# Optimization experiments

Measured on AMD Instinct MI355X. Metric: run time of the kernel, lower is better.

The kernel has to match this reference:

```python
import jax, jax.numpy as jnp
import numpy as np

# ---- batched 6-qubit state-vector simulator ----

def _apply_b(state, gate, wire):
    # per-sample gate: gate (B,2,2), state (B,)+(2,)*w
    B = state.shape[0]; w = state.ndim - 1
    pre = 2 ** wire; post = 2 ** (w - wire - 1)
    s = state.reshape(B, pre, 2, post)
    s = jnp.einsum('bij,bpjq->bpiq', gate, s)
    return s.reshape(state.shape)

def _apply_s(state, gate, wire):
    # shared gate: gate (2,2)
    B = state.shape[0]; w = state.ndim - 1
    pre = 2 ** wire; post = 2 ** (w - wire - 1)
    s = state.reshape(B, pre, 2, post)
    s = jnp.einsum('ij,bpjq->bpiq', gate, s)
    return s.reshape(state.shape)

def _cnot(state, ctrl, tgt):
    s0 = jnp.take(state, 0, axis=1 + ctrl)
    s1 = jnp.take(state, 1, axis=1 + ctrl)
    t_ax = 1 + tgt if tgt < ctrl else tgt  # target axis after removing ctrl axis
    s1 = jnp.flip(s1, axis=t_ax)
    return jnp.stack([s0, s1], axis=1 + ctrl)

def _ry(t):
    c = jnp.cos(t / 2); s = jnp.sin(t / 2)
    return jnp.stack([jnp.stack([c, -s], -1), jnp.stack([s, c], -1)], -2).astype(jnp.complex64)

def _rz(t):
    e = jnp.exp(-0.5j * t.astype(jnp.complex64))
    z = jnp.zeros_like(e)
    return jnp.stack([jnp.stack([e, z], -1), jnp.stack([z, jnp.conj(e)], -1)], -2)

def _rx(t):
    c = jnp.cos(t / 2).astype(jnp.complex64)
    s = (-1j * jnp.sin(t / 2)).astype(jnp.complex64)
    return jnp.stack([jnp.stack([c, s], -1), jnp.stack([s, c], -1)], -2)

def _expvals_z(state):
    p = state.real ** 2 + state.imag ** 2  # (B,)+(2,)*w probabilities
    w = state.ndim - 1
    outs = []
    for i in range(w):
        axes = tuple(a for a in range(1, w + 1) if a != i + 1)
        m = p.sum(axis=axes)  # (B,2) marginal on wire i
        outs.append(m[:, 0] - m[:, 1])
    return jnp.stack(outs, axis=1)  # (B, w) -- matches torch.stack(outputs).T

def _circuit(x, weights):
    # x: (B, w) rescaled features, weights: (layers, 3*w)
    B, w = x.shape
    layers = weights.shape[0]
    e1 = jnp.arctan(x)        # featue_function_1
    e2 = jnp.arctan(x * x)    # featue_function_2 ('atan' type)
    state = jnp.zeros((B,) + (2,) * w, jnp.complex64).at[(slice(None),) + (0,) * w].set(1.0)
    for i in range(w):
        state = _apply_b(state, _ry(e1[:, i]), i)  # AngleEmbedding rotation='Y'
    for i in range(w):
        state = _apply_b(state, _rz(e2[:, i]), i)  # AngleEmbedding rotation='Z'
    for l in range(layers):
        for i in range(w):
            state = _cnot(state, i, (i + 1) % w)
        for i in range(w):
            state = _cnot(state, i, (i + 2) % w)
        for i in range(w):
            state = _apply_s(state, _rx(weights[l, 3 * i + 0]), i)
            state = _apply_s(state, _ry(weights[l, 3 * i + 1]), i)
            state = _apply_s(state, _rz(weights[l, 3 * i + 2]), i)
    return _expvals_z(state)

def _forward(x, phi, Wc, bc):
    Bsz = x.shape[0]
    w = Wc.shape[0]
    sig = jax.nn.sigmoid

    def step(carry, x_t):
        c, h = carry
        z = jnp.concatenate([x_t, h], axis=1)          # torch.hstack([input[:,i], h])
        X = 2.0 * sig(z @ Wc.T + bc) - 1.0             # feature_combiner + rescale
        f_t = sig(_circuit(X, phi[0]))
        i_t = sig(_circuit(X, phi[1]))
        C_t = sig(_circuit(X, phi[2]))
        o_t = sig(_circuit(X, phi[3]))
        c_new = f_t * c + i_t * C_t
        rescaled = o_t * jnp.tanh(c_new)
        h_new = _circuit(rescaled, phi[4])
        y_t = _circuit(rescaled, phi[5])
        return (c_new, h_new), y_t

    init = (jnp.zeros((Bsz, w), jnp.float32), jnp.zeros((Bsz, w), jnp.float32))
    (c, h), ys = jax.lax.scan(jax.checkpoint(step), init, jnp.swapaxes(x, 0, 1))
    return jnp.swapaxes(ys, 0, 1), c, h  # y_out (B,T,w), (c, h)

def setup_inputs() -> dict:
    key = jax.random.key(0)
    k1, k2, k3, k4 = jax.random.split(key, 4)
    x = jax.random.normal(k1, (512, 256, 8), jnp.float32)
    phi = jax.random.normal(k2, (6, 2, 18), jnp.float32) / jnp.sqrt(jnp.float32(2.0))  # std 1/sqrt(layers)
    bound = float(1.0 / np.sqrt(8 + 6))  # Linear(feature_dim+wires, wires) default init
    Wc = jax.random.uniform(k3, (6, 14), jnp.float32, -bound, bound)
    bc = jax.random.uniform(k4, (6,), jnp.float32, -bound, bound)
    return {"x": x, "phi": phi, "Wc": Wc, "bc": bc}

def reference(x, phi, Wc, bc):
    return _forward(x, phi, Wc, bc)
```

## Files before the change

### kernel.cpp

```cpp
#include <hip/hip_runtime.h>


namespace {

constexpr int BATCH  = 512;
constexpr int TSTEPS = 256;

typedef float v2f __attribute__((ext_vector_type(2)));

__device__ __forceinline__ v2f splat2(float s) { v2f r; r.x = s; r.y = s; return r; }
__device__ __forceinline__ v2f cswapneg(v2f v) { v2f r; r.x = -v.y; r.y = v.x; return r; }

__device__ __forceinline__ float sigf(float v) { return 1.0f / (1.0f + __expf(-v)); }
__device__ __forceinline__ float tanh_fast(float v) { return 1.0f - 2.0f / (1.0f + __expf(v + v)); }

__device__ __forceinline__ float rl(float v, int l) {
  return __int_as_float(__builtin_amdgcn_readlane(__float_as_int(v), l));
}

template<int CTRL>
__device__ __forceinline__ float dppmov(float v) {
  return __int_as_float(__builtin_amdgcn_mov_dpp(__float_as_int(v), CTRL, 0xF, 0xF, true));
}

template<int M>
__device__ __forceinline__ float shx(float v, int lane4) {
  if constexpr      (M == 0x01) return dppmov<0xB1>(v);
  else if constexpr (M == 0x02) return dppmov<0x4E>(v);
  else if constexpr (M == 0x03) return dppmov<0x1B>(v);
  else if constexpr (M == 0x04) return dppmov<0x1B>(dppmov<0x141>(v));
  else if constexpr (M == 0x05) return dppmov<0x4E>(dppmov<0x141>(v));
  else if constexpr (M == 0x07) return dppmov<0x141>(v);
  else if constexpr (M == 0x08) return dppmov<0x128>(v);
  else if constexpr (M == 0x0A) return dppmov<0x4E>(dppmov<0x128>(v));
  else if constexpr (M == 0x0C) return dppmov<0x1B>(dppmov<0x140>(v));
  else if constexpr (M == 0x0F) return dppmov<0x140>(v);
  else if constexpr (M < 32) {
    return __int_as_float(__builtin_amdgcn_ds_swizzle(__float_as_int(v), 0x1F | (M << 10)));
  } else {
    return __int_as_float(__builtin_amdgcn_ds_bpermute(lane4 ^ (M << 2), __float_as_int(v)));
  }
}

template<int M>
__device__ __forceinline__ void gate1(v2f& s, float4 A, int pm, int lane4) {
  v2f v; v.x = shx<M>(s.x, lane4); v.y = shx<M>(s.y, lane4);
  float sai = __int_as_float(__float_as_int(A.y) ^ pm);
  float sbr = __int_as_float(__float_as_int(A.z) ^ pm);
  v2f u = splat2(A.x) * s;
  u = __builtin_elementwise_fma(splat2(sai), cswapneg(s), u);
  u = __builtin_elementwise_fma(splat2(sbr), v,           u);
  u = __builtin_elementwise_fma(splat2(A.w), cswapneg(v), u);
  s = u;
}

__device__ __forceinline__ void gate_chain(v2f& s, const float4 (&CA)[12],
                                           const int (&pm)[12], int lane4) {
  gate1<0x0F>(s, CA[0],  pm[0],  lane4);
  gate1<0x1E>(s, CA[1],  pm[1],  lane4);
  gate1<0x3C>(s, CA[2],  pm[2],  lane4);
  gate1<0x3B>(s, CA[3],  pm[3],  lane4);
  gate1<0x3F>(s, CA[4],  pm[4],  lane4);
  gate1<0x3D>(s, CA[5],  pm[5],  lane4);
  gate1<0x16>(s, CA[6],  pm[6],  lane4);
  gate1<0x26>(s, CA[7],  pm[7],  lane4);
  gate1<0x05>(s, CA[8],  pm[8],  lane4);
  gate1<0x28>(s, CA[9],  pm[9],  lane4);
  gate1<0x14>(s, CA[10], pm[10], lane4);
  gate1<0x0A>(s, CA[11], pm[11], lane4);
}

__device__ __forceinline__ float expvals(v2f s, const float (&fs)[9],
                                         int lane4, int gaddr) {
  float p  = fmaf(s.x, s.x, s.y * s.y);
  float pa = shx<1>(p, lane4), pb = shx<2>(p, lane4), pc = shx<3>(p, lane4);
  p = fmaf(fs[0], p, fmaf(fs[1], pa, fmaf(fs[2], pb, pc)));
  pa = shx<4>(p, lane4); pb = shx<8>(p, lane4); pc = shx<12>(p, lane4);
  p = fmaf(fs[3], p, fmaf(fs[4], pa, fmaf(fs[5], pb, pc)));
  pa = shx<16>(p, lane4); pb = shx<32>(p, lane4); pc = shx<48>(p, lane4);
  p = fmaf(fs[6], p, fmaf(fs[7], pa, fmaf(fs[8], pb, pc)));
  return __int_as_float(__builtin_amdgcn_ds_bpermute(gaddr, __float_as_int(p)));
}

__device__ __forceinline__ void trig(float Xv, float& A_, float& B_, float& C_, float& D_) {
  float tq   = Xv * Xv;
  float cth1 = rsqrtf(1.f + tq);
  float sth1 = Xv * cth1;
  float u1   = 1.f + cth1, r1 = rsqrtf(u1 + u1);
  float c1   = u1 * r1,    s1 = sth1 * r1;
  float tq2  = tq * tq;
  float cth2 = rsqrtf(1.f + tq2);
  float sth2 = tq * cth2;
  float u2   = 1.f + cth2, r2 = rsqrtf(u2 + u2);
  float c2   = u2 * r2,    s2 = sth2 * r2;
  A_ = c1 * c2; B_ = c1 * s2; C_ = s1 * c2; D_ = s1 * s2;
}

__device__ __forceinline__ v2f embed_rl(float A_, float B_, float C_, float D_, int lane) {
  float ar, ai;
  {
    float Aj = rl(A_,0), Bj = rl(B_,0), Cj = rl(C_,0), Dj = rl(D_,0);
    bool bj = lane & 1;
    ar = bj ? Cj : Aj;
    ai = bj ? Dj : -Bj;
  }
#pragma unroll
  for (int jj = 1; jj < 6; ++jj) {
    float Aj = rl(A_,jj), Bj = rl(B_,jj), Cj = rl(C_,jj), Dj = rl(D_,jj);
    bool bj = (lane >> jj) & 1;
    float fr = bj ? Cj : Aj;
    float fi = bj ? Dj : -Bj;
    float nr = ar * fr - ai * fi;
    ai = fmaf(ar, fi, ai * fr);
    ar = nr;
  }
  v2f s; s.x = ar; s.y = ai; return s;
}

#define PACK_IDX ((0x2AULL)|(0x15ULL<<6)|(0x01ULL<<12)|(0x35ULL<<18)|(0x3AULL<<24)|(0x3DULL<<30))
#define PIN4(v) asm volatile("" : "+v"((v).x), "+v"((v).y), "+v"((v).z), "+v"((v).w))

}

__global__ __attribute__((amdgpu_flat_work_group_size(256, 256)))
           __attribute__((amdgpu_waves_per_eu(2, 2)))
void qlstm_kernel(const float* __restrict__ x, const float* __restrict__ phi,
                  const float* __restrict__ Wc, const float* __restrict__ bc,
                  float* __restrict__ out)
{
  __shared__ float4 fG[72];
  __shared__ float4 gates4[6];
  __shared__ __align__(16) float h_s[8];

  const int tid   = threadIdx.x;
  const int wave  = tid >> 6;
  const int lane  = tid & 63;
  const int lane4 = lane << 2;
  const int b     = blockIdx.x;

  if (tid < 72) {
    int g = tid / 12, rem = tid % 12, l = rem / 6, i = rem % 6;
    const float* w = phi + g*36 + l*18 + i*3;
    float sa, ca, sb, cb, sc, cc;
    sincosf(0.5f * w[0], &sa, &ca);
    sincosf(0.5f * w[1], &sb, &cb);
    sincosf(0.5f * w[2], &sc, &cc);
    float m00r =  cb*ca, m00i =  sb*sa;
    float m01r = -sb*ca, m01i = -cb*sa;
    float4 A;
    A.x = m00r*cc + m00i*sc;  A.y = m00i*cc - m00r*sc;
    A.z = m01r*cc + m01i*sc;  A.w = m01i*cc - m01r*sc;
    fG[tid] = A;
  }
  if (tid < 8) h_s[tid] = 0.f;
  __syncthreads();

  const int j = (lane < 6) ? lane : 0;
  float Wr[14];
#pragma unroll
  for (int k = 0; k < 14; ++k) Wr[k] = Wc[j*14 + k];
  const float bcj = bc[j];

  float sgn[6];
#pragma unroll
  for (int k = 0; k < 6; ++k) sgn[k] = ((lane >> k) & 1) ? -1.f : 1.f;
  float fs[9] = { sgn[0]*sgn[1], sgn[1], sgn[0],
                  sgn[2]*sgn[3], sgn[3], sgn[2],
                  sgn[4]*sgn[5], sgn[5], sgn[4] };

  int sh    = (lane < 6) ? (6 * lane) : 0;
  int gaddr = (int)((PACK_IDX >> sh) & 63ULL) << 2;

  constexpr unsigned BM[2][6] = {
    {0x18,0x30,0x39,0x0C,0x26,0x33},
    {0x2A,0x15,0x01,0x35,0x3A,0x3D}};
  int pm[12];
#pragma unroll
  for (int l = 0; l < 2; ++l)
#pragma unroll
    for (int i = 0; i < 6; ++i)
      pm[l*6+i] = (__popc(lane & (int)BM[l][i]) & 1) << 31;
#pragma unroll
  for (int g = 0; g < 12; ++g) asm volatile("" : "+v"(pm[g]));

  float4 CA1[12], CA2[12];
#pragma unroll
  for (int i = 0; i < 12; ++i) {
    CA1[i] = fG[wave * 12 + i];
    CA2[i] = fG[(4 + (wave & 1)) * 12 + i];
  }
#pragma unroll
  for (int i = 0; i < 12; ++i) { PIN4(CA1[i]); PIN4(CA2[i]); }

  float c_sc  = 0.f;
  float hlast = 0.f;

  const float* xbase = x + (size_t)b * TSTEPS * 8;
  float4 xa = *(const float4*)(xbase);
  float4 xb = *(const float4*)(xbase + 4);

  for (int t = 0; t < TSTEPS; ++t) {
    float4 h4 = *(const float4*)&h_s[0];
    float2 h2 = *(const float2*)&h_s[4];
    float acc = bcj;
    acc = fmaf(xa.x, Wr[0],  acc); acc = fmaf(xa.y, Wr[1],  acc);
    acc = fmaf(xa.z, Wr[2],  acc); acc = fmaf(xa.w, Wr[3],  acc);
    acc = fmaf(xb.x, Wr[4],  acc); acc = fmaf(xb.y, Wr[5],  acc);
    acc = fmaf(xb.z, Wr[6],  acc); acc = fmaf(xb.w, Wr[7],  acc);
    acc = fmaf(h4.x, Wr[8],  acc); acc = fmaf(h4.y, Wr[9],  acc);
    acc = fmaf(h4.z, Wr[10], acc); acc = fmaf(h4.w, Wr[11], acc);
    acc = fmaf(h2.x, Wr[12], acc); acc = fmaf(h2.y, Wr[13], acc);
    float Xj = 1.f - 2.f / (1.f + __expf(acc));

    int tn = (t + 1 < TSTEPS) ? (t + 1) : t;
    float4 xa_n = *(const float4*)(xbase + (size_t)tn * 8);
    float4 xb_n = *(const float4*)(xbase + (size_t)tn * 8 + 4);

    float A_, B_, C_, D_;
    trig(Xj, A_, B_, C_, D_);
    v2f s = embed_rl(A_, B_, C_, D_, lane);
    gate_chain(s, CA1, pm, lane4);
    float Wv  = expvals(s, fs, lane4, gaddr);
    float sgv = sigf(Wv);
    if (lane < 6) ((float*)&gates4[lane])[wave] = sgv;
    __syncthreads();

    if (wave < 2) {
      float4 g4 = gates4[j];
      float cn  = fmaf(g4.x, c_sc, g4.y * g4.z);
      c_sc = cn;
      float resc = g4.w * tanh_fast(cn);
      float A2, B2, C2, D2;
      trig(resc, A2, B2, C2, D2);
      v2f s2 = embed_rl(A2, B2, C2, D2, lane);
      gate_chain(s2, CA2, pm, lane4);
      float Wv2 = expvals(s2, fs, lane4, gaddr);
      if (wave == 0) {
        if (lane < 6) h_s[lane] = Wv2;
        hlast = Wv2;
      } else if (lane < 6) {
        out[((size_t)b * TSTEPS + t) * 6 + lane] = Wv2;
      }
    }
    xa = xa_n; xb = xb_n;
    __syncthreads();
  }

  if (wave == 0 && lane < 6) {
    size_t cbase = (size_t)BATCH * TSTEPS * 6;
    out[cbase + (size_t)b * 6 + lane] = c_sc;
    out[cbase + (size_t)BATCH * 6 + (size_t)b * 6 + lane] = hlast;
  }
}

extern "C" void kernel_launch(void* const* d_in, const int* in_sizes, int n_in,
                              void* d_out, int out_size, void* d_ws, size_t ws_size,
                              hipStream_t stream) {
  const float* x   = (const float*)d_in[0];
  const float* phi = (const float*)d_in[1];
  const float* Wc  = (const float*)d_in[2];
  const float* bc  = (const float*)d_in[3];
  float* out = (float*)d_out;
  (void)in_sizes; (void)n_in; (void)out_size; (void)d_ws; (void)ws_size;
  hipLaunchKernelGGL(qlstm_kernel, dim3(BATCH), dim3(256), 0, stream,
                     x, phi, Wc, bc, out);
}
```

Baseline: 622.6 us.

## Run all six circuits per sample in one wave with interleaved gate chains

Each batch element now uses a single 64-lane wavefront instead of four waves. That wave runs the four gate circuits interleaved (N=4), then the two output circuits interleaved (N=2). Gate coefficients are read from LDS in a gate-major layout, and the hidden state stays in registers and is broadcast with readlane. This removes the two block-wide barriers and the LDS exchange per timestep, and gives the scheduler independent chains to hide shuffle latency. In exchange each wave does all six circuits serially, only 512 waves run in total, and coefficients are reloaded from LDS every step instead of held pinned in registers.

```diff
diff --git a/kernel.cpp b/kernel.cpp
--- a/kernel.cpp
+++ b/kernel.cpp
@@ -42,44 +42,71 @@
   }
 }
 
-template<int M>
-__device__ __forceinline__ void gate1(v2f& s, float4 A, int pm, int lane4) {
-  v2f v; v.x = shx<M>(s.x, lane4); v.y = shx<M>(s.y, lane4);
-  float sai = __int_as_float(__float_as_int(A.y) ^ pm);
-  float sbr = __int_as_float(__float_as_int(A.z) ^ pm);
-  v2f u = splat2(A.x) * s;
-  u = __builtin_elementwise_fma(splat2(sai), cswapneg(s), u);
-  u = __builtin_elementwise_fma(splat2(sbr), v,           u);
-  u = __builtin_elementwise_fma(splat2(A.w), cswapneg(v), u);
-  s = u;
-}
-
-__device__ __forceinline__ void gate_chain(v2f& s, const float4 (&CA)[12],
-                                           const int (&pm)[12], int lane4) {
-  gate1<0x0F>(s, CA[0],  pm[0],  lane4);
-  gate1<0x1E>(s, CA[1],  pm[1],  lane4);
-  gate1<0x3C>(s, CA[2],  pm[2],  lane4);
-  gate1<0x3B>(s, CA[3],  pm[3],  lane4);
-  gate1<0x3F>(s, CA[4],  pm[4],  lane4);
-  gate1<0x3D>(s, CA[5],  pm[5],  lane4);
-  gate1<0x16>(s, CA[6],  pm[6],  lane4);
-  gate1<0x26>(s, CA[7],  pm[7],  lane4);
-  gate1<0x05>(s, CA[8],  pm[8],  lane4);
-  gate1<0x28>(s, CA[9],  pm[9],  lane4);
-  gate1<0x14>(s, CA[10], pm[10], lane4);
-  gate1<0x0A>(s, CA[11], pm[11], lane4);
-}
-
-__device__ __forceinline__ float expvals(v2f s, const float (&fs)[9],
-                                         int lane4, int gaddr) {
-  float p  = fmaf(s.x, s.x, s.y * s.y);
-  float pa = shx<1>(p, lane4), pb = shx<2>(p, lane4), pc = shx<3>(p, lane4);
-  p = fmaf(fs[0], p, fmaf(fs[1], pa, fmaf(fs[2], pb, pc)));
-  pa = shx<4>(p, lane4); pb = shx<8>(p, lane4); pc = shx<12>(p, lane4);
-  p = fmaf(fs[3], p, fmaf(fs[4], pa, fmaf(fs[5], pb, pc)));
-  pa = shx<16>(p, lane4); pb = shx<32>(p, lane4); pc = shx<48>(p, lane4);
-  p = fmaf(fs[6], p, fmaf(fs[7], pa, fmaf(fs[8], pb, pc)));
-  return __int_as_float(__builtin_amdgcn_ds_bpermute(gaddr, __float_as_int(p)));
+template<int M, int N>
+__device__ __forceinline__ void gateN(v2f (&s)[N], const float4* __restrict__ Ks,
+                                      int pm, int lane4) {
+  float4 A[N];
+#pragma unroll
+  for (int c = 0; c < N; ++c) A[c] = Ks[c];
+  v2f v[N];
+#pragma unroll
+  for (int c = 0; c < N; ++c) {
+    v[c].x = shx<M>(s[c].x, lane4);
+    v[c].y = shx<M>(s[c].y, lane4);
+  }
+#pragma unroll
+  for (int c = 0; c < N; ++c) {
+    float sai = __int_as_float(__float_as_int(A[c].y) ^ pm);
+    float sbr = __int_as_float(__float_as_int(A[c].z) ^ pm);
+    v2f u = splat2(A[c].x) * s[c];
+    u = __builtin_elementwise_fma(splat2(sai), cswapneg(s[c]), u);
+    u = __builtin_elementwise_fma(splat2(sbr), v[c],           u);
+    u = __builtin_elementwise_fma(splat2(A[c].w), cswapneg(v[c]), u);
+    s[c] = u;
+  }
+}
+
+template<int N>
+__device__ __forceinline__ void chainN(v2f (&s)[N], const float4* __restrict__ Kt,
+                                       int base, const int (&pm)[12], int lane4) {
+  gateN<0x0F, N>(s, Kt + 0*6  + base, pm[0],  lane4);
+  gateN<0x1E, N>(s, Kt + 1*6  + base, pm[1],  lane4);
+  gateN<0x3C, N>(s, Kt + 2*6  + base, pm[2],  lane4);
+  gateN<0x3B, N>(s, Kt + 3*6  + base, pm[3],  lane4);
+  gateN<0x3F, N>(s, Kt + 4*6  + base, pm[4],  lane4);
+  gateN<0x3D, N>(s, Kt + 5*6  + base, pm[5],  lane4);
+  gateN<0x16, N>(s, Kt + 6*6  + base, pm[6],  lane4);
+  gateN<0x26, N>(s, Kt + 7*6  + base, pm[7],  lane4);
+  gateN<0x05, N>(s, Kt + 8*6  + base, pm[8],  lane4);
+  gateN<0x28, N>(s, Kt + 9*6  + base, pm[9],  lane4);
+  gateN<0x14, N>(s, Kt + 10*6 + base, pm[10], lane4);
+  gateN<0x0A, N>(s, Kt + 11*6 + base, pm[11], lane4);
+}
+
+template<int N>
+__device__ __forceinline__ void expvalsN(const v2f (&s)[N], float (&Wv)[N],
+                                         const float (&fs)[9], int lane4, int gaddr) {
+  float p[N];
+#pragma unroll
+  for (int c = 0; c < N; ++c) p[c] = fmaf(s[c].x, s[c].x, s[c].y * s[c].y);
+#pragma unroll
+  for (int c = 0; c < N; ++c) {
+    float pa = shx<1>(p[c], lane4), pb = shx<2>(p[c], lane4), pc = shx<3>(p[c], lane4);
+    p[c] = fmaf(fs[0], p[c], fmaf(fs[1], pa, fmaf(fs[2], pb, pc)));
+  }
+#pragma unroll
+  for (int c = 0; c < N; ++c) {
+    float pa = shx<4>(p[c], lane4), pb = shx<8>(p[c], lane4), pc = shx<12>(p[c], lane4);
+    p[c] = fmaf(fs[3], p[c], fmaf(fs[4], pa, fmaf(fs[5], pb, pc)));
+  }
+#pragma unroll
+  for (int c = 0; c < N; ++c) {
+    float pa = shx<16>(p[c], lane4), pb = shx<32>(p[c], lane4), pc = shx<48>(p[c], lane4);
+    p[c] = fmaf(fs[6], p[c], fmaf(fs[7], pa, fmaf(fs[8], pb, pc)));
+  }
+#pragma unroll
+  for (int c = 0; c < N; ++c)
+    Wv[c] = __int_as_float(__builtin_amdgcn_ds_bpermute(gaddr, __float_as_int(p[c])));
 }
 
 __device__ __forceinline__ void trig(float Xv, float& A_, float& B_, float& C_, float& D_) {
@@ -118,28 +145,22 @@
 }
 
 #define PACK_IDX ((0x2AULL)|(0x15ULL<<6)|(0x01ULL<<12)|(0x35ULL<<18)|(0x3AULL<<24)|(0x3DULL<<30))
-#define PIN4(v) asm volatile("" : "+v"((v).x), "+v"((v).y), "+v"((v).z), "+v"((v).w))
-
-}
-
-__global__ __attribute__((amdgpu_flat_work_group_size(256, 256)))
-           __attribute__((amdgpu_waves_per_eu(2, 2)))
+
+}
+
+__global__ __launch_bounds__(64) __attribute__((amdgpu_waves_per_eu(1)))
 void qlstm_kernel(const float* __restrict__ x, const float* __restrict__ phi,
                   const float* __restrict__ Wc, const float* __restrict__ bc,
                   float* __restrict__ out)
 {
-  __shared__ float4 fG[72];
-  __shared__ float4 gates4[6];
-  __shared__ __align__(16) float h_s[8];
-
-  const int tid   = threadIdx.x;
-  const int wave  = tid >> 6;
-  const int lane  = tid & 63;
+  __shared__ float4 Kt[72];
+
+  const int lane  = threadIdx.x & 63;
   const int lane4 = lane << 2;
   const int b     = blockIdx.x;
 
-  if (tid < 72) {
-    int g = tid / 12, rem = tid % 12, l = rem / 6, i = rem % 6;
+  for (int k = lane; k < 72; k += 64) {
+    int g = k / 12, rem = k % 12, l = rem / 6, i = rem % 6;
     const float* w = phi + g*36 + l*18 + i*3;
     float sa, ca, sb, cb, sc, cc;
     sincosf(0.5f * w[0], &sa, &ca);
@@ -150,9 +171,8 @@
     float4 A;
     A.x = m00r*cc + m00i*sc;  A.y = m00i*cc - m00r*sc;
     A.z = m01r*cc + m01i*sc;  A.w = m01i*cc - m01r*sc;
-    fG[tid] = A;
-  }
-  if (tid < 8) h_s[tid] = 0.f;
+    Kt[rem*6 + g] = A;
+  }
   __syncthreads();
 
   const int j = (lane < 6) ? lane : 0;
@@ -180,36 +200,25 @@
 #pragma unroll
     for (int i = 0; i < 6; ++i)
       pm[l*6+i] = (__popc(lane & (int)BM[l][i]) & 1) << 31;
-#pragma unroll
-  for (int g = 0; g < 12; ++g) asm volatile("" : "+v"(pm[g]));
-
-  float4 CA1[12], CA2[12];
-#pragma unroll
-  for (int i = 0; i < 12; ++i) {
-    CA1[i] = fG[wave * 12 + i];
-    CA2[i] = fG[(4 + (wave & 1)) * 12 + i];
-  }
-#pragma unroll
-  for (int i = 0; i < 12; ++i) { PIN4(CA1[i]); PIN4(CA2[i]); }
-
-  float c_sc  = 0.f;
-  float hlast = 0.f;
+
+  float c_sc = 0.f;
+  float hreg = 0.f;
 
   const float* xbase = x + (size_t)b * TSTEPS * 8;
   float4 xa = *(const float4*)(xbase);
   float4 xb = *(const float4*)(xbase + 4);
 
   for (int t = 0; t < TSTEPS; ++t) {
-    float4 h4 = *(const float4*)&h_s[0];
-    float2 h2 = *(const float2*)&h_s[4];
+    float h0 = rl(hreg,0), h1 = rl(hreg,1), h2 = rl(hreg,2);
+    float h3 = rl(hreg,3), h4 = rl(hreg,4), h5 = rl(hreg,5);
     float acc = bcj;
     acc = fmaf(xa.x, Wr[0],  acc); acc = fmaf(xa.y, Wr[1],  acc);
     acc = fmaf(xa.z, Wr[2],  acc); acc = fmaf(xa.w, Wr[3],  acc);
     acc = fmaf(xb.x, Wr[4],  acc); acc = fmaf(xb.y, Wr[5],  acc);
     acc = fmaf(xb.z, Wr[6],  acc); acc = fmaf(xb.w, Wr[7],  acc);
-    acc = fmaf(h4.x, Wr[8],  acc); acc = fmaf(h4.y, Wr[9],  acc);
-    acc = fmaf(h4.z, Wr[10], acc); acc = fmaf(h4.w, Wr[11], acc);
-    acc = fmaf(h2.x, Wr[12], acc); acc = fmaf(h2.y, Wr[13], acc);
+    acc = fmaf(h0,   Wr[8],  acc); acc = fmaf(h1,   Wr[9],  acc);
+    acc = fmaf(h2,   Wr[10], acc); acc = fmaf(h3,   Wr[11], acc);
+    acc = fmaf(h4,   Wr[12], acc); acc = fmaf(h5,   Wr[13], acc);
     float Xj = 1.f - 2.f / (1.f + __expf(acc));
 
     int tn = (t + 1 < TSTEPS) ? (t + 1) : t;
@@ -218,38 +227,36 @@
 
     float A_, B_, C_, D_;
     trig(Xj, A_, B_, C_, D_);
-    v2f s = embed_rl(A_, B_, C_, D_, lane);
-    gate_chain(s, CA1, pm, lane4);
-    float Wv  = expvals(s, fs, lane4, gaddr);
-    float sgv = sigf(Wv);
-    if (lane < 6) ((float*)&gates4[lane])[wave] = sgv;
-    __syncthreads();
-
-    if (wave < 2) {
-      float4 g4 = gates4[j];
-      float cn  = fmaf(g4.x, c_sc, g4.y * g4.z);
-      c_sc = cn;
-      float resc = g4.w * tanh_fast(cn);
-      float A2, B2, C2, D2;
-      trig(resc, A2, B2, C2, D2);
-      v2f s2 = embed_rl(A2, B2, C2, D2, lane);
-      gate_chain(s2, CA2, pm, lane4);
-      float Wv2 = expvals(s2, fs, lane4, gaddr);
-      if (wave == 0) {
-        if (lane < 6) h_s[lane] = Wv2;
-        hlast = Wv2;
-      } else if (lane < 6) {
-        out[((size_t)b * TSTEPS + t) * 6 + lane] = Wv2;
-      }
-    }
+    v2f e = embed_rl(A_, B_, C_, D_, lane);
+    v2f s4[4] = { e, e, e, e };
+    chainN<4>(s4, Kt, 0, pm, lane4);
+    float Wv[4];
+    expvalsN<4>(s4, Wv, fs, lane4, gaddr);
+
+    float fg = sigf(Wv[0]), ig = sigf(Wv[1]);
+    float Cg = sigf(Wv[2]), og = sigf(Wv[3]);
+    float cn = fmaf(fg, c_sc, ig * Cg);
+    c_sc = cn;
+    float resc = og * tanh_fast(cn);
+
+    float A2, B2, C2, D2;
+    trig(resc, A2, B2, C2, D2);
+    v2f e2 = embed_rl(A2, B2, C2, D2, lane);
+    v2f s2[2] = { e2, e2 };
+    chainN<2>(s2, Kt, 4, pm, lane4);
+    float Wv2[2];
+    expvalsN<2>(s2, Wv2, fs, lane4, gaddr);
+
+    hreg = Wv2[0];
+    if (lane < 6) out[((size_t)b * TSTEPS + t) * 6 + lane] = Wv2[1];
+
     xa = xa_n; xb = xb_n;
-    __syncthreads();
-  }
-
-  if (wave == 0 && lane < 6) {
+  }
+
+  if (lane < 6) {
     size_t cbase = (size_t)BATCH * TSTEPS * 6;
     out[cbase + (size_t)b * 6 + lane] = c_sc;
-    out[cbase + (size_t)BATCH * 6 + (size_t)b * 6 + lane] = hlast;
+    out[cbase + (size_t)BATCH * 6 + (size_t)b * 6 + lane] = hreg;
   }
 }
 
@@ -262,6 +269,6 @@
   const float* bc  = (const float*)d_in[3];
   float* out = (float*)d_out;
   (void)in_sizes; (void)n_in; (void)out_size; (void)d_ws; (void)ws_size;
-  hipLaunchKernelGGL(qlstm_kernel, dim3(BATCH), dim3(256), 0, stream,
+  hipLaunchKernelGGL(qlstm_kernel, dim3(BATCH), dim3(64), 0, stream,
                      x, phi, Wc, bc, out);
 }
```

Measured after the change: 1.997 ms. +220.8%, slower.

## Drop final bpermute, build embedding as product tree, precompute gate coefficients

Applied to the files above, without the earlier changes.

Each sample's wire-j result is now read straight from the lane that already holds the reduced expectation, so the final ds_bpermute in expv goes away. Gate indices move to those specific lanes (gidx). The product-state embedding is built as a balanced tree of complex multiplies instead of a serial chain, which shortens the dependency chain. Gate matrices are computed once in a small prep kernel into workspace instead of in every block, at the cost of an extra launch and of dropping the register-pinning asm.

```diff
diff --git a/kernel.cpp b/kernel.cpp
--- a/kernel.cpp
+++ b/kernel.cpp
@@ -10,6 +10,9 @@
 
 __device__ __forceinline__ v2f splat2(float s) { v2f r; r.x = s; r.y = s; return r; }
 __device__ __forceinline__ v2f cswapneg(v2f v) { v2f r; r.x = -v.y; r.y = v.x; return r; }
+__device__ __forceinline__ v2f cmul(v2f a, v2f b) {
+  v2f r; r.x = fmaf(a.x, b.x, -(a.y * b.y)); r.y = fmaf(a.x, b.y, a.y * b.x); return r;
+}
 
 __device__ __forceinline__ float sigf(float v) { return 1.0f / (1.0f + __expf(-v)); }
 __device__ __forceinline__ float tanh_fast(float v) { return 1.0f - 2.0f / (1.0f + __expf(v + v)); }
@@ -54,24 +57,23 @@
   s = u;
 }
 
-__device__ __forceinline__ void gate_chain(v2f& s, const float4 (&CA)[12],
-                                           const int (&pm)[12], int lane4) {
-  gate1<0x0F>(s, CA[0],  pm[0],  lane4);
-  gate1<0x1E>(s, CA[1],  pm[1],  lane4);
-  gate1<0x3C>(s, CA[2],  pm[2],  lane4);
-  gate1<0x3B>(s, CA[3],  pm[3],  lane4);
-  gate1<0x3F>(s, CA[4],  pm[4],  lane4);
-  gate1<0x3D>(s, CA[5],  pm[5],  lane4);
-  gate1<0x16>(s, CA[6],  pm[6],  lane4);
-  gate1<0x26>(s, CA[7],  pm[7],  lane4);
-  gate1<0x05>(s, CA[8],  pm[8],  lane4);
-  gate1<0x28>(s, CA[9],  pm[9],  lane4);
-  gate1<0x14>(s, CA[10], pm[10], lane4);
-  gate1<0x0A>(s, CA[11], pm[11], lane4);
-}
-
-__device__ __forceinline__ float expvals(v2f s, const float (&fs)[9],
-                                         int lane4, int gaddr) {
+__device__ __forceinline__ void chain12(v2f& s, const float4 (&K)[12],
+                                        const int (&pm)[12], int lane4) {
+  gate1<0x0F>(s, K[0],  pm[0],  lane4);
+  gate1<0x1E>(s, K[1],  pm[1],  lane4);
+  gate1<0x3C>(s, K[2],  pm[2],  lane4);
+  gate1<0x3B>(s, K[3],  pm[3],  lane4);
+  gate1<0x3F>(s, K[4],  pm[4],  lane4);
+  gate1<0x3D>(s, K[5],  pm[5],  lane4);
+  gate1<0x16>(s, K[6],  pm[6],  lane4);
+  gate1<0x26>(s, K[7],  pm[7],  lane4);
+  gate1<0x05>(s, K[8],  pm[8],  lane4);
+  gate1<0x28>(s, K[9],  pm[9],  lane4);
+  gate1<0x14>(s, K[10], pm[10], lane4);
+  gate1<0x0A>(s, K[11], pm[11], lane4);
+}
+
+__device__ __forceinline__ float expv(v2f s, const float (&fs)[9], int lane4) {
   float p  = fmaf(s.x, s.x, s.y * s.y);
   float pa = shx<1>(p, lane4), pb = shx<2>(p, lane4), pc = shx<3>(p, lane4);
   p = fmaf(fs[0], p, fmaf(fs[1], pa, fmaf(fs[2], pb, pc)));
@@ -79,7 +81,7 @@
   p = fmaf(fs[3], p, fmaf(fs[4], pa, fmaf(fs[5], pb, pc)));
   pa = shx<16>(p, lane4); pb = shx<32>(p, lane4); pc = shx<48>(p, lane4);
   p = fmaf(fs[6], p, fmaf(fs[7], pa, fmaf(fs[8], pb, pc)));
-  return __int_as_float(__builtin_amdgcn_ds_bpermute(gaddr, __float_as_int(p)));
+  return p;
 }
 
 __device__ __forceinline__ void trig(float Xv, float& A_, float& B_, float& C_, float& D_) {
@@ -96,50 +98,29 @@
   A_ = c1 * c2; B_ = c1 * s2; C_ = s1 * c2; D_ = s1 * s2;
 }
 
-__device__ __forceinline__ v2f embed_rl(float A_, float B_, float C_, float D_, int lane) {
-  float ar, ai;
-  {
-    float Aj = rl(A_,0), Bj = rl(B_,0), Cj = rl(C_,0), Dj = rl(D_,0);
-    bool bj = lane & 1;
-    ar = bj ? Cj : Aj;
-    ai = bj ? Dj : -Bj;
-  }
-#pragma unroll
-  for (int jj = 1; jj < 6; ++jj) {
-    float Aj = rl(A_,jj), Bj = rl(B_,jj), Cj = rl(C_,jj), Dj = rl(D_,jj);
-    bool bj = (lane >> jj) & 1;
-    float fr = bj ? Cj : Aj;
-    float fi = bj ? Dj : -Bj;
-    float nr = ar * fr - ai * fi;
-    ai = fmaf(ar, fi, ai * fr);
-    ar = nr;
-  }
-  v2f s; s.x = ar; s.y = ai; return s;
-}
-
-#define PACK_IDX ((0x2AULL)|(0x15ULL<<6)|(0x01ULL<<12)|(0x35ULL<<18)|(0x3AULL<<24)|(0x3DULL<<30))
-#define PIN4(v) asm volatile("" : "+v"((v).x), "+v"((v).y), "+v"((v).z), "+v"((v).w))
-
-}
-
-__global__ __attribute__((amdgpu_flat_work_group_size(256, 256)))
-           __attribute__((amdgpu_waves_per_eu(2, 2)))
-void qlstm_kernel(const float* __restrict__ x, const float* __restrict__ phi,
-                  const float* __restrict__ Wc, const float* __restrict__ bc,
-                  float* __restrict__ out)
-{
-  __shared__ float4 fG[72];
-  __shared__ float4 gates4[6];
-  __shared__ __align__(16) float h_s[8];
-
-  const int tid   = threadIdx.x;
-  const int wave  = tid >> 6;
-  const int lane  = tid & 63;
-  const int lane4 = lane << 2;
-  const int b     = blockIdx.x;
-
-  if (tid < 72) {
-    int g = tid / 12, rem = tid % 12, l = rem / 6, i = rem % 6;
+__device__ __forceinline__ v2f embed_tree(float A_, float B_, float C_, float D_, int lane) {
+  constexpr int LW[6] = {0x2A, 0x15, 0x01, 0x35, 0x3A, 0x3D};
+  v2f f[6];
+#pragma unroll
+  for (int w = 0; w < 6; ++w) {
+    float Aj = rl(A_, LW[w]), Bj = rl(B_, LW[w]);
+    float Cj = rl(C_, LW[w]), Dj = rl(D_, LW[w]);
+    bool bj = (lane >> w) & 1;
+    f[w].x = bj ? Cj : Aj;
+    f[w].y = bj ? Dj : -Bj;
+  }
+  v2f p01 = cmul(f[0], f[1]);
+  v2f p23 = cmul(f[2], f[3]);
+  v2f p45 = cmul(f[4], f[5]);
+  return cmul(cmul(p01, p23), p45);
+}
+
+}
+
+__global__ void qlstm_prep(const float* __restrict__ phi, float4* __restrict__ Kw) {
+  int k = threadIdx.x;
+  if (k < 72) {
+    int g = k / 12, rem = k % 12, l = rem / 6, i = rem % 6;
     const float* w = phi + g*36 + l*18 + i*3;
     float sa, ca, sb, cb, sc, cc;
     sincosf(0.5f * w[0], &sa, &ca);
@@ -150,16 +131,42 @@
     float4 A;
     A.x = m00r*cc + m00i*sc;  A.y = m00i*cc - m00r*sc;
     A.z = m01r*cc + m01i*sc;  A.w = m01i*cc - m01r*sc;
-    fG[tid] = A;
-  }
+    Kw[g*12 + rem] = A;
+  }
+}
+
+__global__ __launch_bounds__(256, 2)
+void qlstm_kernel(const float* __restrict__ x, const float* __restrict__ Wc,
+                  const float* __restrict__ bc, const float4* __restrict__ Kw,
+                  float* __restrict__ out)
+{
+  __shared__ float4 gates4[6];
+  __shared__ __align__(16) float h_s[8];
+
+  const int tid   = threadIdx.x;
+  const int wave  = tid >> 6;
+  const int lane  = tid & 63;
+  const int lane4 = lane << 2;
+  const int b     = blockIdx.x;
+
   if (tid < 8) h_s[tid] = 0.f;
-  __syncthreads();
-
-  const int j = (lane < 6) ? lane : 0;
+
+  const int c1off = __builtin_amdgcn_readfirstlane(wave * 12);
+  const int c2off = __builtin_amdgcn_readfirstlane((4 + (wave & 1)) * 12);
+  float4 K1[12], K2[12];
+#pragma unroll
+  for (int i = 0; i < 12; ++i) K1[i] = Kw[c1off + i];
+#pragma unroll
+  for (int i = 0; i < 12; ++i) K2[i] = Kw[c2off + i];
+
+  const int gidx = (lane == 0x2A) ? 0 : (lane == 0x15) ? 1 : (lane == 0x01) ? 2 :
+                   (lane == 0x35) ? 3 : (lane == 0x3A) ? 4 : (lane == 0x3D) ? 5 : -1;
+  const int jrow = (gidx >= 0) ? gidx : 0;
+
   float Wr[14];
 #pragma unroll
-  for (int k = 0; k < 14; ++k) Wr[k] = Wc[j*14 + k];
-  const float bcj = bc[j];
+  for (int k = 0; k < 14; ++k) Wr[k] = Wc[jrow*14 + k];
+  const float bcj = bc[jrow];
 
   float sgn[6];
 #pragma unroll
@@ -168,9 +175,6 @@
                   sgn[2]*sgn[3], sgn[3], sgn[2],
                   sgn[4]*sgn[5], sgn[5], sgn[4] };
 
-  int sh    = (lane < 6) ? (6 * lane) : 0;
-  int gaddr = (int)((PACK_IDX >> sh) & 63ULL) << 2;
-
   constexpr unsigned BM[2][6] = {
     {0x18,0x30,0x39,0x0C,0x26,0x33},
     {0x2A,0x15,0x01,0x35,0x3A,0x3D}};
@@ -180,17 +184,6 @@
 #pragma unroll
     for (int i = 0; i < 6; ++i)
       pm[l*6+i] = (__popc(lane & (int)BM[l][i]) & 1) << 31;
-#pragma unroll
-  for (int g = 0; g < 12; ++g) asm volatile("" : "+v"(pm[g]));
-
-  float4 CA1[12], CA2[12];
-#pragma unroll
-  for (int i = 0; i < 12; ++i) {
-    CA1[i] = fG[wave * 12 + i];
-    CA2[i] = fG[(4 + (wave & 1)) * 12 + i];
-  }
-#pragma unroll
-  for (int i = 0; i < 12; ++i) { PIN4(CA1[i]); PIN4(CA2[i]); }
 
   float c_sc  = 0.f;
   float hlast = 0.f;
@@ -198,6 +191,8 @@
   const float* xbase = x + (size_t)b * TSTEPS * 8;
   float4 xa = *(const float4*)(xbase);
   float4 xb = *(const float4*)(xbase + 4);
+
+  __syncthreads();
 
   for (int t = 0; t < TSTEPS; ++t) {
     float4 h4 = *(const float4*)&h_s[0];
@@ -218,38 +213,38 @@
 
     float A_, B_, C_, D_;
     trig(Xj, A_, B_, C_, D_);
-    v2f s = embed_rl(A_, B_, C_, D_, lane);
-    gate_chain(s, CA1, pm, lane4);
-    float Wv  = expvals(s, fs, lane4, gaddr);
-    float sgv = sigf(Wv);
-    if (lane < 6) ((float*)&gates4[lane])[wave] = sgv;
+    v2f s = embed_tree(A_, B_, C_, D_, lane);
+    chain12(s, K1, pm, lane4);
+    float p   = expv(s, fs, lane4);
+    float sgv = sigf(p);
+    if (gidx >= 0) ((float*)&gates4[gidx])[wave] = sgv;
     __syncthreads();
 
     if (wave < 2) {
-      float4 g4 = gates4[j];
+      float4 g4 = gates4[jrow];
       float cn  = fmaf(g4.x, c_sc, g4.y * g4.z);
       c_sc = cn;
       float resc = g4.w * tanh_fast(cn);
       float A2, B2, C2, D2;
       trig(resc, A2, B2, C2, D2);
-      v2f s2 = embed_rl(A2, B2, C2, D2, lane);
-      gate_chain(s2, CA2, pm, lane4);
-      float Wv2 = expvals(s2, fs, lane4, gaddr);
+      v2f s2 = embed_tree(A2, B2, C2, D2, lane);
+      chain12(s2, K2, pm, lane4);
+      float p2v = expv(s2, fs, lane4);
       if (wave == 0) {
-        if (lane < 6) h_s[lane] = Wv2;
-        hlast = Wv2;
-      } else if (lane < 6) {
-        out[((size_t)b * TSTEPS + t) * 6 + lane] = Wv2;
+        if (gidx >= 0) h_s[gidx] = p2v;
+        hlast = p2v;
+      } else if (gidx >= 0) {
+        out[((size_t)b * TSTEPS + t) * 6 + gidx] = p2v;
       }
     }
     xa = xa_n; xb = xb_n;
     __syncthreads();
   }
 
-  if (wave == 0 && lane < 6) {
+  if (wave == 0 && gidx >= 0) {
     size_t cbase = (size_t)BATCH * TSTEPS * 6;
-    out[cbase + (size_t)b * 6 + lane] = c_sc;
-    out[cbase + (size_t)BATCH * 6 + (size_t)b * 6 + lane] = hlast;
+    out[cbase + (size_t)b * 6 + gidx] = c_sc;
+    out[cbase + (size_t)BATCH * 6 + (size_t)b * 6 + gidx] = hlast;
   }
 }
 
@@ -261,7 +256,9 @@
   const float* Wc  = (const float*)d_in[2];
   const float* bc  = (const float*)d_in[3];
   float* out = (float*)d_out;
-  (void)in_sizes; (void)n_in; (void)out_size; (void)d_ws; (void)ws_size;
+  float4* Kw = (float4*)d_ws;
+  (void)in_sizes; (void)n_in; (void)out_size; (void)ws_size;
+  hipLaunchKernelGGL(qlstm_prep, dim3(1), dim3(128), 0, stream, phi, Kw);
   hipLaunchKernelGGL(qlstm_kernel, dim3(BATCH), dim3(256), 0, stream,
-                     x, phi, Wc, bc, out);
-}
+                     x, Wc, bc, Kw, out);
+}
```

After: 679.6 us. 1.09x slower.
